# Optimization experiments

Measured on AMD Instinct MI355X. Metric: run time of the kernel, lower is better.

The kernel has to match this reference:

```python
import jax, jax.numpy as jnp
import numpy as np
from jax import lax

K_NN = 16      # neighbors used by compute_knn_distance
ANCHOR_K = 64  # config['anchor_k']


def _knn_dist_vec(pts):
    """compute_knn_distance for one object: mean offset vector to K_NN nearest neighbors.
    pts: (N, 3) -> (N, 3)"""
    sq = jnp.sum(pts * pts, axis=-1)                      # (N,)
    d2 = sq[:, None] + sq[None, :] - 2.0 * (pts @ pts.T)  # (N, N) squared dists
    n = pts.shape[0]
    d2 = d2 + jnp.eye(n, dtype=pts.dtype) * 1e10          # exclude self
    _, idx = lax.top_k(-d2, K_NN)                          # (N, K_NN) nearest indices
    neigh = pts[idx]                                       # (N, K_NN, 3)
    return jnp.mean(neigh - pts[:, None, :], axis=1)       # (N, 3)


def _fps(pts, k):
    """Farthest point sampling for one object. pts: (N, 3) -> (k,) int32 indices."""
    d0 = jnp.sum((pts - pts[0]) ** 2, axis=-1)             # dist to seed point 0

    def step(min_d, _):
        idx = jnp.argmax(min_d)
        d = jnp.sum((pts - pts[idx]) ** 2, axis=-1)
        return jnp.minimum(min_d, d), idx

    _, idxs = lax.scan(step, d0, None, length=k - 1)
    return jnp.concatenate([jnp.zeros((1,), dtype=idxs.dtype), idxs])


def setup_inputs() -> dict:
    key = jax.random.key(0)
    k1, k2, k3, k4 = jax.random.split(key, 4)
    B, N_obj, N_v = 4, 8, 2048
    positions = jax.random.normal(k1, (B, N_obj, N_v, 3), dtype=jnp.float32)
    velocities = jax.random.normal(k2, (B, N_obj, N_v, 3), dtype=jnp.float32)
    physics_params = jax.random.uniform(k3, (B, N_obj, 3), dtype=jnp.float32)
    # reference pose at t=0: nearby but distinct so rel_pos is nontrivial
    ref_positions = positions + 0.05 * jax.random.normal(k4, (B, N_obj, N_v, 3), dtype=jnp.float32)
    return {"positions": positions, "velocities": velocities,
            "physics_params": physics_params, "ref_positions": ref_positions}


def reference(positions, velocities, physics_params, ref_positions):
    B, N_obj, N_v, _ = positions.shape
    flat = positions.reshape(B * N_obj, N_v, 3)

    # pairwise KNN distance feature per point
    dist_vec = jax.vmap(_knn_dist_vec)(flat).reshape(B, N_obj, N_v, 3)

    # iterative FPS anchor sampling (vectorized over all B*N_obj objects)
    anchors = jax.vmap(lambda p: _fps(p, ANCHOR_K))(flat).reshape(B, N_obj, ANCHOR_K)

    rel_pos = positions - ref_positions

    # multi-field gather at anchor indices (torch.gather on dim=2)
    gather = lambda f: jnp.take_along_axis(f, anchors[..., None], axis=2)
    anchor_dist = gather(dist_vec)       # (B, N_obj, K, 3)
    anchor_vel = gather(velocities)      # (B, N_obj, K, 3)
    anchor_rel = gather(rel_pos)         # (B, N_obj, K, 3)

    phys = jnp.broadcast_to(physics_params[:, :, None, :], (B, N_obj, ANCHOR_K, 3))
    query = jnp.concatenate([anchor_dist, anchor_vel, anchor_rel, phys], axis=-1)  # (B, N_obj, K, 12)
    return query
```

## Files before the change

kernel.cpp:

```cpp
#include <hip/hip_runtime.h>
#include <stdint.h>

#define NPTS 2048
#define KNN  16
#define AK   64
#define TPB  256
#define FPT  (NPTS / TPB)
#define KPL  (NPTS / 64)

typedef unsigned long long u64;
typedef unsigned int u32;
typedef unsigned short u16;
#define UMAX 0xFFFFFFFFFFFFFFFFull

__device__ __forceinline__ float sq3(float x, float y, float z) {
    return __fadd_rn(__fadd_rn(__fmul_rn(x, x), __fmul_rn(y, y)), __fmul_rn(z, z));
}

template <int CTRL>
__device__ __forceinline__ u64 dpp64(u64 k) {
    const int lo = __builtin_amdgcn_update_dpp((int)(u32)k, (int)(u32)k,
                                               CTRL, 0xF, 0xF, false);
    const int hi = __builtin_amdgcn_update_dpp((int)(u32)(k >> 32),
                                               (int)(u32)(k >> 32),
                                               CTRL, 0xF, 0xF, false);
    return ((u64)(u32)hi << 32) | (u32)lo;
}

__device__ __forceinline__ void swap16_pair(u64 k, u64& a, u64& b) {
#if __has_builtin(__builtin_amdgcn_permlane16_swap)
    const u32 lo = (u32)k, hi = (u32)(k >> 32);
    const auto rl = __builtin_amdgcn_permlane16_swap(lo, lo, false, false);
    const auto rh = __builtin_amdgcn_permlane16_swap(hi, hi, false, false);
    a = ((u64)(u32)rh[0] << 32) | (u32)rl[0];
    b = ((u64)(u32)rh[1] << 32) | (u32)rl[1];
#else
    a = (u64)__shfl_xor((long long)k, 16, 64);
    b = a;
#endif
}

__device__ __forceinline__ void swap32_pair(u64 k, u64& a, u64& b) {
#if __has_builtin(__builtin_amdgcn_permlane32_swap)
    const u32 lo = (u32)k, hi = (u32)(k >> 32);
    const auto rl = __builtin_amdgcn_permlane32_swap(lo, lo, false, false);
    const auto rh = __builtin_amdgcn_permlane32_swap(hi, hi, false, false);
    a = ((u64)(u32)rh[0] << 32) | (u32)rl[0];
    b = ((u64)(u32)rh[1] << 32) | (u32)rl[1];
#else
    a = (u64)__shfl_xor((long long)k, 32, 64);
    b = a;
#endif
}

__device__ __forceinline__ u64 wave_max64(u64 k) {
    u64 o, a, b;
    o = dpp64<0xB1>(k);  if (o > k) k = o;
    o = dpp64<0x4E>(k);  if (o > k) k = o;
    o = dpp64<0x141>(k); if (o > k) k = o;
    o = dpp64<0x140>(k); if (o > k) k = o;
    swap16_pair(k, a, b); if (a > k) k = a; if (b > k) k = b;
    swap32_pair(k, a, b); if (a > k) k = a; if (b > k) k = b;
    return k;
}

__device__ __forceinline__ u64 wave_min64(u64 k) {
    u64 o, a, b;
    o = dpp64<0xB1>(k);  if (o < k) k = o;
    o = dpp64<0x4E>(k);  if (o < k) k = o;
    o = dpp64<0x141>(k); if (o < k) k = o;
    o = dpp64<0x140>(k); if (o < k) k = o;
    swap16_pair(k, a, b); if (a < k) k = a; if (b < k) k = b;
    swap32_pair(k, a, b); if (a < k) k = a; if (b < k) k = b;
    return k;
}

__global__ __launch_bounds__(TPB) void fused_kernel(
    const float* __restrict__ pos, const float* __restrict__ vel,
    const float* __restrict__ phys, const float* __restrict__ refp,
    u64* __restrict__ aq, float* __restrict__ out, int n_obj) {
    const int b = blockIdx.x;
    const int t = threadIdx.x;
    const int wid = t >> 6, lane = t & 63;

    __shared__ float4 sP[NPTS];
    __shared__ u64 skey[8];
    __shared__ float4 scrd[8];
    __shared__ u64 sQ;

    if (b < n_obj) {
        const int obj = b;
        const float* pts = pos + (size_t)obj * NPTS * 3;
        float px[FPT], py[FPT], pz[FPT], mind[FPT];
        #pragma unroll
        for (int i = 0; i < FPT; i++) {
            const int j = t + i * TPB;
            const float x = pts[j * 3 + 0];
            const float y = pts[j * 3 + 1];
            const float z = pts[j * 3 + 2];
            px[i] = x; py[i] = y; pz[i] = z;
            sP[j] = make_float4(x, y, z, 0.f);
        }
        __syncthreads();

        u64 qacc = 0;
        #define PUSH_AID(v) qacc = (qacc >> 16) | ((u64)(u16)(v) << 48)
        PUSH_AID(0);

        u64 key;
        {
            const float4 c0 = sP[0];
            float bv = -1.0f; u32 bj = 0;
            #pragma unroll
            for (int i = 0; i < FPT; i++) {
                const float d2 = sq3(__fsub_rn(px[i], c0.x), __fsub_rn(py[i], c0.y),
                                     __fsub_rn(pz[i], c0.z));
                mind[i] = d2;
                if (d2 > bv) { bv = d2; bj = (u32)(t + i * TPB); }
            }
            key = ((u64)__float_as_uint(bv) << 32) | (u32)(~bj);
        }

        #pragma unroll 1
        for (int s = 1; s < AK; s++) {
            const u64 wk = wave_max64(key);
            const int side = (s & 1) * 4;
            if (lane == 0) {
                const int widx = (int)(~(u32)wk);
                skey[side + wid] = wk;
                scrd[side + wid] = sP[widx];
            }
            __syncthreads();
            u64 ka = skey[side + 0];
            float4 ca = scrd[side + 0];
            { const u64 k1 = skey[side + 1]; const float4 q = scrd[side + 1];
              if (k1 > ka) { ka = k1; ca = q; } }
            { const u64 k2 = skey[side + 2]; const float4 q = scrd[side + 2];
              if (k2 > ka) { ka = k2; ca = q; } }
            { const u64 k3 = skey[side + 3]; const float4 q = scrd[side + 3];
              if (k3 > ka) { ka = k3; ca = q; } }

            PUSH_AID((int)(~(u32)ka));
            if ((s & 3) == 3 && t == 0) {
                __hip_atomic_store(&aq[obj * 16 + (s >> 2)], qacc,
                                   __ATOMIC_RELAXED, __HIP_MEMORY_SCOPE_AGENT);
            }
            if (s == AK - 1) break;

            float bv = -1.0f; u32 bj = 0;
            #pragma unroll
            for (int i = 0; i < FPT; i++) {
                const float d2 = sq3(__fsub_rn(px[i], ca.x), __fsub_rn(py[i], ca.y),
                                     __fsub_rn(pz[i], ca.z));
                const float nm = fminf(mind[i], d2);
                mind[i] = nm;
                if (nm > bv) { bv = nm; bj = (u32)(t + i * TPB); }
            }
            key = ((u64)__float_as_uint(bv) << 32) | (u32)(~bj);
        }
        return;
    }

    const int g4 = b - n_obj;
    const int obj = g4 >> 4;
    const int q = g4 & 15;
    const int g = obj * AK + q * 4 + wid;

    const float* pts = pos + (size_t)obj * NPTS * 3;
    #pragma unroll
    for (int i = 0; i < FPT; i++) {
        const int j = t + i * TPB;
        const float x = pts[j * 3 + 0];
        const float y = pts[j * 3 + 1];
        const float z = pts[j * 3 + 2];
        sP[j] = make_float4(x, y, z, sq3(x, y, z));
    }
    if (t == 0) {
        u64 v;
        for (;;) {
            v = __hip_atomic_load(&aq[obj * 16 + q], __ATOMIC_RELAXED,
                                  __HIP_MEMORY_SCOPE_AGENT);
            if (v != 0) break;
            __builtin_amdgcn_s_sleep(2);
        }
        sQ = v;
    }
    __syncthreads();
    const int a = (int)((sQ >> (16 * wid)) & 0xFFFF);

    const float4 ca = sP[a];
    const float ax = ca.x, ay = ca.y, az = ca.z;
    const float sqa = ca.w;

    u64 k[KPL];
    #pragma unroll
    for (int i = 0; i < KPL; i++) {
        const int j = lane + i * 64;
        const float4 p = sP[j];
        const float dot = __fadd_rn(
            __fadd_rn(__fmul_rn(ax, p.x), __fmul_rn(ay, p.y)), __fmul_rn(az, p.z));
        const float d2 = __fsub_rn(__fadd_rn(sqa, p.w), __fmul_rn(2.0f, dot));
        u32 bb = __float_as_uint(d2);
        bb ^= (bb & 0x80000000u) ? 0xFFFFFFFFu : 0x80000000u;
        k[i] = (j == a) ? UMAX : (((u64)bb << 32) | (u32)j);
    }

    u64 c0 = UMAX, c1 = UMAX, c2 = UMAX, c3 = UMAX;
    #pragma unroll
    for (int i = 0; i < KPL; i++) c0 = (k[i] < c0) ? k[i] : c0;
    #pragma unroll
    for (int i = 0; i < KPL; i++) {
        const u64 v = (k[i] > c0) ? k[i] : UMAX; c1 = (v < c1) ? v : c1;
    }
    #pragma unroll
    for (int i = 0; i < KPL; i++) {
        const u64 v = (k[i] > c1) ? k[i] : UMAX; c2 = (v < c2) ? v : c2;
    }
    #pragma unroll
    for (int i = 0; i < KPL; i++) {
        const u64 v = (k[i] > c2) ? k[i] : UMAX; c3 = (v < c3) ? v : c3;
    }

    float accx = 0.f, accy = 0.f, accz = 0.f;
    u64 thr = 0;
    float4 cw;
    {
        const u64 w = wave_min64(c0);
        cw = sP[(int)(u32)w];
        if (c0 == w) { thr = c0; c0 = c1; c1 = c2; c2 = c3; c3 = UMAX; }
    }
    #pragma unroll 1
    for (int r = 1; r < KNN; r++) {
        if (c0 == UMAX) {
            #pragma unroll
            for (int i = 0; i < KPL; i++) {
                const u64 v = (k[i] > thr) ? k[i] : UMAX; c0 = (v < c0) ? v : c0;
            }
            #pragma unroll
            for (int i = 0; i < KPL; i++) {
                const u64 v = (k[i] > c0) ? k[i] : UMAX; c1 = (v < c1) ? v : c1;
            }
            #pragma unroll
            for (int i = 0; i < KPL; i++) {
                const u64 v = (k[i] > c1) ? k[i] : UMAX; c2 = (v < c2) ? v : c2;
            }
            #pragma unroll
            for (int i = 0; i < KPL; i++) {
                const u64 v = (k[i] > c2) ? k[i] : UMAX; c3 = (v < c3) ? v : c3;
            }
        }
        const u64 w = wave_min64(c0);
        const float4 cn = sP[(int)(u32)w];
        accx = __fadd_rn(accx, __fsub_rn(cw.x, ax));
        accy = __fadd_rn(accy, __fsub_rn(cw.y, ay));
        accz = __fadd_rn(accz, __fsub_rn(cw.z, az));
        cw = cn;
        if (c0 == w) {
            thr = c0; c0 = c1; c1 = c2; c2 = c3; c3 = UMAX;
        }
    }
    accx = __fadd_rn(accx, __fsub_rn(cw.x, ax));
    accy = __fadd_rn(accy, __fsub_rn(cw.y, ay));
    accz = __fadd_rn(accz, __fsub_rn(cw.z, az));

    if (lane == 0) {
        float* o = out + (size_t)g * 12;
        o[0] = __fmul_rn(accx, 0.0625f);
        o[1] = __fmul_rn(accy, 0.0625f);
        o[2] = __fmul_rn(accz, 0.0625f);
        const size_t base = (size_t)obj * NPTS * 3 + (size_t)a * 3;
        o[3] = vel[base + 0];
        o[4] = vel[base + 1];
        o[5] = vel[base + 2];
        o[6] = __fsub_rn(pos[base + 0], refp[base + 0]);
        o[7] = __fsub_rn(pos[base + 1], refp[base + 1]);
        o[8] = __fsub_rn(pos[base + 2], refp[base + 2]);
        const float* ph = phys + (size_t)obj * 3;
        o[9]  = ph[0];
        o[10] = ph[1];
        o[11] = ph[2];
    }
}

extern "C" void kernel_launch(void* const* d_in, const int* in_sizes, int n_in,
                              void* d_out, int out_size, void* d_ws, size_t ws_size,
                              hipStream_t stream) {
    const float* pos  = (const float*)d_in[0];
    const float* vel  = (const float*)d_in[1];
    const float* phys = (const float*)d_in[2];
    const float* refp = (const float*)d_in[3];
    float* out = (float*)d_out;

    const int n_obj = in_sizes[2] / 3;
    u64* aq = (u64*)d_ws;

    hipMemsetAsync(aq, 0, (size_t)n_obj * 16 * sizeof(u64), stream);

    fused_kernel<<<n_obj * 17, TPB, 0, stream>>>(pos, vel, phys, refp,
                                                 aq, out, n_obj);
}
```

Baseline: 106.6 us.

## Run last anchor group's KNN in FPS block and use lighter LDS barrier

Each FPS block now keeps the last four anchor indices in registers and runs their KNN work itself. Before, a separate consumer block had to wait on a global flag for that final group, so the tail of the critical path gets shorter and the grid shrinks by one block per object. The FPS loop swaps __syncthreads for a bare lgkmcnt wait plus s_barrier, and the consumer spin-sleep is lengthened. The KNN code is moved into a shared inline function. The cost is a longer FPS block: it now does a full KNN pass after the scan, and the division by 15 costs a little more than the old shift.

```diff
diff --git a/kernel.cpp b/kernel.cpp
--- a/kernel.cpp
+++ b/kernel.cpp
@@ -16,6 +16,12 @@
 __device__ __forceinline__ float sq3(float x, float y, float z) {
     return __fadd_rn(__fadd_rn(__fmul_rn(x, x), __fmul_rn(y, y)), __fmul_rn(z, z));
 }
+
+#define BAR_LDS() do {                                        \
+    asm volatile("s_waitcnt lgkmcnt(0)" ::: "memory");        \
+    __builtin_amdgcn_s_barrier();                             \
+    asm volatile("" ::: "memory");                            \
+} while (0)
 
 template <int CTRL>
 __device__ __forceinline__ u64 dpp64(u64 k) {
@@ -75,119 +81,11 @@
     return k;
 }
 
-__global__ __launch_bounds__(TPB) void fused_kernel(
+__device__ __forceinline__ void knn_body(
+    const float4* __restrict__ sP, int a, int g, int obj, int lane,
     const float* __restrict__ pos, const float* __restrict__ vel,
     const float* __restrict__ phys, const float* __restrict__ refp,
-    u64* __restrict__ aq, float* __restrict__ out, int n_obj) {
-    const int b = blockIdx.x;
-    const int t = threadIdx.x;
-    const int wid = t >> 6, lane = t & 63;
-
-    __shared__ float4 sP[NPTS];
-    __shared__ u64 skey[8];
-    __shared__ float4 scrd[8];
-    __shared__ u64 sQ;
-
-    if (b < n_obj) {
-        const int obj = b;
-        const float* pts = pos + (size_t)obj * NPTS * 3;
-        float px[FPT], py[FPT], pz[FPT], mind[FPT];
-        #pragma unroll
-        for (int i = 0; i < FPT; i++) {
-            const int j = t + i * TPB;
-            const float x = pts[j * 3 + 0];
-            const float y = pts[j * 3 + 1];
-            const float z = pts[j * 3 + 2];
-            px[i] = x; py[i] = y; pz[i] = z;
-            sP[j] = make_float4(x, y, z, 0.f);
-        }
-        __syncthreads();
-
-        u64 qacc = 0;
-        #define PUSH_AID(v) qacc = (qacc >> 16) | ((u64)(u16)(v) << 48)
-        PUSH_AID(0);
-
-        u64 key;
-        {
-            const float4 c0 = sP[0];
-            float bv = -1.0f; u32 bj = 0;
-            #pragma unroll
-            for (int i = 0; i < FPT; i++) {
-                const float d2 = sq3(__fsub_rn(px[i], c0.x), __fsub_rn(py[i], c0.y),
-                                     __fsub_rn(pz[i], c0.z));
-                mind[i] = d2;
-                if (d2 > bv) { bv = d2; bj = (u32)(t + i * TPB); }
-            }
-            key = ((u64)__float_as_uint(bv) << 32) | (u32)(~bj);
-        }
-
-        #pragma unroll 1
-        for (int s = 1; s < AK; s++) {
-            const u64 wk = wave_max64(key);
-            const int side = (s & 1) * 4;
-            if (lane == 0) {
-                const int widx = (int)(~(u32)wk);
-                skey[side + wid] = wk;
-                scrd[side + wid] = sP[widx];
-            }
-            __syncthreads();
-            u64 ka = skey[side + 0];
-            float4 ca = scrd[side + 0];
-            { const u64 k1 = skey[side + 1]; const float4 q = scrd[side + 1];
-              if (k1 > ka) { ka = k1; ca = q; } }
-            { const u64 k2 = skey[side + 2]; const float4 q = scrd[side + 2];
-              if (k2 > ka) { ka = k2; ca = q; } }
-            { const u64 k3 = skey[side + 3]; const float4 q = scrd[side + 3];
-              if (k3 > ka) { ka = k3; ca = q; } }
-
-            PUSH_AID((int)(~(u32)ka));
-            if ((s & 3) == 3 && t == 0) {
-                __hip_atomic_store(&aq[obj * 16 + (s >> 2)], qacc,
-                                   __ATOMIC_RELAXED, __HIP_MEMORY_SCOPE_AGENT);
-            }
-            if (s == AK - 1) break;
-
-            float bv = -1.0f; u32 bj = 0;
-            #pragma unroll
-            for (int i = 0; i < FPT; i++) {
-                const float d2 = sq3(__fsub_rn(px[i], ca.x), __fsub_rn(py[i], ca.y),
-                                     __fsub_rn(pz[i], ca.z));
-                const float nm = fminf(mind[i], d2);
-                mind[i] = nm;
-                if (nm > bv) { bv = nm; bj = (u32)(t + i * TPB); }
-            }
-            key = ((u64)__float_as_uint(bv) << 32) | (u32)(~bj);
-        }
-        return;
-    }
-
-    const int g4 = b - n_obj;
-    const int obj = g4 >> 4;
-    const int q = g4 & 15;
-    const int g = obj * AK + q * 4 + wid;
-
-    const float* pts = pos + (size_t)obj * NPTS * 3;
-    #pragma unroll
-    for (int i = 0; i < FPT; i++) {
-        const int j = t + i * TPB;
-        const float x = pts[j * 3 + 0];
-        const float y = pts[j * 3 + 1];
-        const float z = pts[j * 3 + 2];
-        sP[j] = make_float4(x, y, z, sq3(x, y, z));
-    }
-    if (t == 0) {
-        u64 v;
-        for (;;) {
-            v = __hip_atomic_load(&aq[obj * 16 + q], __ATOMIC_RELAXED,
-                                  __HIP_MEMORY_SCOPE_AGENT);
-            if (v != 0) break;
-            __builtin_amdgcn_s_sleep(2);
-        }
-        sQ = v;
-    }
-    __syncthreads();
-    const int a = (int)((sQ >> (16 * wid)) & 0xFFFF);
-
+    float* __restrict__ out) {
     const float4 ca = sP[a];
     const float ax = ca.x, ay = ca.y, az = ca.z;
     const float sqa = ca.w;
@@ -282,6 +180,138 @@
     }
 }
 
+__global__ __launch_bounds__(TPB) void fused_kernel(
+    const float* __restrict__ pos, const float* __restrict__ vel,
+    const float* __restrict__ phys, const float* __restrict__ refp,
+    u64* __restrict__ aq, float* __restrict__ out, int n_obj) {
+    const int b = blockIdx.x;
+    const int t = threadIdx.x;
+    const int wid = t >> 6, lane = t & 63;
+
+    __shared__ float4 sP[NPTS];
+    __shared__ u64 skey[8];
+    __shared__ float4 scrd[8];
+    __shared__ u64 sQ;
+
+    if (b < n_obj) {
+        const int obj = b;
+        const float* pts = pos + (size_t)obj * NPTS * 3;
+        float px[FPT], py[FPT], pz[FPT], mind[FPT];
+        #pragma unroll
+        for (int i = 0; i < FPT; i++) {
+            const int j = t + i * TPB;
+            const float x = pts[j * 3 + 0];
+            const float y = pts[j * 3 + 1];
+            const float z = pts[j * 3 + 2];
+            px[i] = x; py[i] = y; pz[i] = z;
+            sP[j] = make_float4(x, y, z, sq3(x, y, z));
+        }
+        __syncthreads();
+
+        u64 qacc = 0;
+        #define PUSH_AID(v) qacc = (qacc >> 16) | ((u64)(u16)(v) << 48)
+        PUSH_AID(0);
+        u32 pa0 = 0, pa1 = 0, pa2 = 0, pa3 = 0;
+
+        u64 key;
+        {
+            const float4 c0 = sP[0];
+            float bv = -1.0f; u32 bj = 0;
+            #pragma unroll
+            for (int i = 0; i < FPT; i++) {
+                const float d2 = sq3(__fsub_rn(px[i], c0.x), __fsub_rn(py[i], c0.y),
+                                     __fsub_rn(pz[i], c0.z));
+                mind[i] = d2;
+                if (d2 > bv) { bv = d2; bj = (u32)(t + i * TPB); }
+            }
+            key = ((u64)__float_as_uint(bv) << 32) | (u32)(~bj);
+        }
+
+        #pragma unroll 1
+        for (int s = 1; s < AK; s++) {
+            const u64 wk = wave_max64(key);
+            const int side = (s & 1) * 4;
+            if (lane == 0) {
+                const int widx = (int)(~(u32)wk);
+                skey[side + wid] = wk;
+                scrd[side + wid] = sP[widx];
+            }
+            BAR_LDS();
+            u64 ka = skey[side + 0];
+            float4 ca = scrd[side + 0];
+            { const u64 k1 = skey[side + 1]; const float4 qv = scrd[side + 1];
+              if (k1 > ka) { ka = k1; ca = qv; } }
+            { const u64 k2 = skey[side + 2]; const float4 qv = scrd[side + 2];
+              if (k2 > ka) { ka = k2; ca = qv; } }
+            { const u64 k3 = skey[side + 3]; const float4 qv = scrd[side + 3];
+              if (k3 > ka) { ka = k3; ca = qv; } }
+
+            const u32 aid = ~(u32)ka;
+            PUSH_AID(aid);
+            if ((s & 3) == 3 && s < 60 && t == 0) {
+                __hip_atomic_store(&aq[obj * 15 + (s >> 2)], qacc,
+                                   __ATOMIC_RELAXED, __HIP_MEMORY_SCOPE_AGENT);
+            }
+            if (s >= 60) {
+                const int r = s - 60;
+                if (r == 0) pa0 = aid;
+                else if (r == 1) pa1 = aid;
+                else if (r == 2) pa2 = aid;
+                else pa3 = aid;
+            }
+            if (s == AK - 1) break;
+
+            float bv = -1.0f; u32 bj = 0;
+            #pragma unroll
+            for (int i = 0; i < FPT; i++) {
+                const float d2 = sq3(__fsub_rn(px[i], ca.x), __fsub_rn(py[i], ca.y),
+                                     __fsub_rn(pz[i], ca.z));
+                const float nm = fminf(mind[i], d2);
+                mind[i] = nm;
+                if (nm > bv) { bv = nm; bj = (u32)(t + i * TPB); }
+            }
+            key = ((u64)__float_as_uint(bv) << 32) | (u32)(~bj);
+        }
+
+        u32 av = pa0;
+        if (wid == 1) av = pa1;
+        else if (wid == 2) av = pa2;
+        else if (wid == 3) av = pa3;
+        knn_body(sP, (int)av, obj * AK + 60 + wid, obj, lane,
+                 pos, vel, phys, refp, out);
+        return;
+    }
+
+    const int g4 = b - n_obj;
+    const int obj = g4 / 15;
+    const int q = g4 % 15;
+    const int g = obj * AK + q * 4 + wid;
+
+    const float* pts = pos + (size_t)obj * NPTS * 3;
+    #pragma unroll
+    for (int i = 0; i < FPT; i++) {
+        const int j = t + i * TPB;
+        const float x = pts[j * 3 + 0];
+        const float y = pts[j * 3 + 1];
+        const float z = pts[j * 3 + 2];
+        sP[j] = make_float4(x, y, z, sq3(x, y, z));
+    }
+    if (t == 0) {
+        u64 v;
+        for (;;) {
+            v = __hip_atomic_load(&aq[obj * 15 + q], __ATOMIC_RELAXED,
+                                  __HIP_MEMORY_SCOPE_AGENT);
+            if (v != 0) break;
+            __builtin_amdgcn_s_sleep(8);
+        }
+        sQ = v;
+    }
+    __syncthreads();
+    const int a = (int)((sQ >> (16 * wid)) & 0xFFFF);
+
+    knn_body(sP, a, g, obj, lane, pos, vel, phys, refp, out);
+}
+
 extern "C" void kernel_launch(void* const* d_in, const int* in_sizes, int n_in,
                               void* d_out, int out_size, void* d_ws, size_t ws_size,
                               hipStream_t stream) {
@@ -294,8 +324,8 @@
     const int n_obj = in_sizes[2] / 3;
     u64* aq = (u64*)d_ws;
 
-    hipMemsetAsync(aq, 0, (size_t)n_obj * 16 * sizeof(u64), stream);
-
-    fused_kernel<<<n_obj * 17, TPB, 0, stream>>>(pos, vel, phys, refp,
+    hipMemsetAsync(aq, 0, (size_t)n_obj * 15 * sizeof(u64), stream);
+
+    fused_kernel<<<n_obj * 16, TPB, 0, stream>>>(pos, vel, phys, refp,
                                                  aq, out, n_obj);
 }
```

After: 105.5 us. Within noise of the previous version (-1.0%).
